# Kernel tuning notes

Measured on AMD Instinct MI355X. Metric: run time of the kernel, lower is better.

Reference implementation:

```python
import jax, jax.numpy as jnp
import numpy as np

BETA = 0.25


def setup_inputs() -> dict:
    key = jax.random.key(0)
    k1, k2 = jax.random.split(key)
    z = jax.random.normal(k1, (16, 1024, 256), dtype=jnp.float32)
    embedding = jax.random.normal(k2, (8192, 256), dtype=jnp.float32)
    return {"z": z, "embedding": embedding}


def reference(z, embedding):
    e_dim = embedding.shape[-1]
    z_flat = jnp.reshape(z, (-1, e_dim))  # [N, e_dim]
    # d[i,k] = ||z_i||^2 + ||e_k||^2 - 2 z_i . e_k  -> [N, n_e]
    d = (jnp.sum(z_flat ** 2, axis=1, keepdims=True)
         + jnp.sum(embedding ** 2, axis=1)
         - 2.0 * jnp.einsum('nd,kd->nk', z_flat, embedding))
    min_encoding_indices = jnp.argmin(d, axis=1)  # [N]
    z_q = embedding[min_encoding_indices]
    z_q = jnp.reshape(z_q, z.shape)
    loss = (jnp.mean((jax.lax.stop_gradient(z_q) - z) ** 2)
            + BETA * jnp.mean((z_q - jax.lax.stop_gradient(z)) ** 2))
    z_q = z + jax.lax.stop_gradient(z_q - z)  # straight-through estimator
    return (z_q, loss, min_encoding_indices)
```

## Files before the change

kernel.cpp:

```cpp
#include <hip/hip_runtime.h>
#include <stdint.h>

#define N_ROWS   16384
#define DIM      256
#define N_CODES  8192
#define ZQ_ELEMS 4194304

typedef _Float16 f16x8 __attribute__((ext_vector_type(8)));
typedef _Float16 f16x4 __attribute__((ext_vector_type(4)));
typedef float    f32x16 __attribute__((ext_vector_type(16)));
typedef unsigned long long u64;

#define WS_ET  0
#define WS_PK  (8650752)

static __device__ __forceinline__ void glds16(const void* gsrc, void* ldst) {
    __builtin_amdgcn_global_load_lds(
        (const __attribute__((address_space(1))) unsigned int*)gsrc,
        (__attribute__((address_space(3))) unsigned int*)ldst,
        16, 0, 0);
}

static __device__ __forceinline__ u64 packkey(float d, int c) {
    unsigned int u = __float_as_uint(d);
    u ^= ((unsigned int)((int)u >> 31)) | 0x80000000u;
    return ((u64)u << 32) | (unsigned int)c;
}

__global__ void vq_prep(const float* __restrict__ emb, const float* __restrict__ z,
                        _Float16* __restrict__ et, _Float16* __restrict__ zt,
                        float* __restrict__ loss_ptr) {
    __shared__ _Float16 shbuf[32768];
    const int t = threadIdx.x, w = t >> 6, l = t & 63;
    if (blockIdx.x < 2048) {
        if (blockIdx.x == 0 && t == 0) *loss_ptr = 0.0f;
        _Float16 (*lh)[256] = (_Float16(*)[256])shbuf;
        _Float16 (*ll)[256] = (_Float16(*)[256])(shbuf + 1024);
        const int code = blockIdx.x * 4 + w;
        float4 v = *(const float4*)(emb + (size_t)code * DIM + l * 4);
        float xs[4] = {v.x, v.y, v.z, v.w};
        f16x4 hh, lo;
        float s = 0.0f;
        #pragma unroll
        for (int i = 0; i < 4; ++i) {
            _Float16 h = (_Float16)xs[i];
            hh[i] = h;
            lo[i] = (_Float16)(xs[i] - (float)h);
            s += xs[i] * xs[i];
        }
        *(f16x4*)&lh[w][l * 4] = hh;
        *(f16x4*)&ll[w][l * 4] = lo;
        #pragma unroll
        for (int off = 32; off > 0; off >>= 1) s += __shfl_down(s, off, 64);
        if (l == 0) {
            _Float16 nh = (_Float16)s;
            _Float16 nl = (_Float16)(s - (float)nh);
            f16x8 aug, zr;
            #pragma unroll
            for (int i = 0; i < 8; ++i) { aug[i] = (_Float16)0; zr[i] = (_Float16)0; }
            aug[0] = nh; aug[1] = nl;
            *(f16x8*)(et + ((size_t)64 * N_CODES + code) * 8) = aug;
            *(f16x8*)(et + ((size_t)65 * N_CODES + code) * 8) = zr;
        }
        __syncthreads();
        const int p = t >> 7, g = t & 127;
        const int cl = g & 3, fg = g >> 2;
        f16x8 frag = (p == 0) ? *(const f16x8*)&lh[cl][fg * 8]
                              : *(const f16x8*)&ll[cl][fg * 8];
        const size_t slab = (size_t)(p * 32 + fg);
        *(f16x8*)(et + (slab * N_CODES + blockIdx.x * 4 + cl) * 8) = frag;
    } else {
        _Float16 (*ls)[64][256] = (_Float16(*)[64][256])shbuf;
        const int row0 = (blockIdx.x - 2048) * 64;
        #pragma unroll
        for (int j = 0; j < 16; ++j) {
            const int row = w * 16 + j;
            float4 v = *(const float4*)(z + (size_t)(row0 + row) * DIM + l * 4);
            float xs[4] = {v.x, v.y, v.z, v.w};
            f16x4 hh, lo;
            #pragma unroll
            for (int i = 0; i < 4; ++i) {
                const float m2 = -2.0f * xs[i];
                _Float16 h = (_Float16)m2;
                hh[i] = h;
                lo[i] = (_Float16)(m2 - (float)h);
            }
            *(f16x4*)&ls[0][row][l * 4] = hh;
            *(f16x4*)&ls[1][row][l * 4] = lo;
        }
        __syncthreads();
        #pragma unroll
        for (int pass = 0; pass < 16; ++pass) {
            const int slab = pass * 4 + w;
            const int p = slab >> 5, fg = slab & 31;
            f16x8 frag = *(const f16x8*)&ls[p][l][fg * 8];
            *(f16x8*)(zt + ((size_t)slab * N_ROWS + row0 + l) * 8) = frag;
        }
    }
}

__global__ __launch_bounds__(512, 2)
void vq_main(const _Float16* __restrict__ zt, const _Float16* __restrict__ et,
             u64* __restrict__ pkeys) {
    extern __shared__ char smem[];
    _Float16* zs = (_Float16*)smem;
    u64* run = (u64*)(smem + 131072);

    const int tid = threadIdx.x;
    const int w = tid >> 6, L = tid & 63, lo5 = L & 31, hi1 = L >> 5;
    const int rb = blockIdx.x >> 1, sp = blockIdx.x & 1;
    const int row0 = rb * 128, codeS = sp * 4096;

    #pragma unroll
    for (int i = 0; i < 16; ++i) {
        const int idx = w * 16 + i;
        const int slab = idx >> 1, half = idx & 1;
        glds16(zt + ((size_t)slab * N_ROWS + row0 + half * 64 + L) * 8,
               smem + ((slab * 128 + half * 64 + L) << 4));
    }
    run[tid] = ~0ULL;
    run[tid + 512] = ~0ULL;
    __syncthreads();

    f16x8 bz;
    #pragma unroll
    for (int i = 0; i < 8; ++i) bz[i] = (_Float16)0;
    if (hi1 == 0) { bz[0] = (_Float16)1; bz[1] = (_Float16)1; }

    for (int ci = 0; ci < 8; ++ci) {
        const int c0 = codeS + ci * 512 + w * 64;

        f16x8 paug[2];
        #pragma unroll
        for (int mt = 0; mt < 2; ++mt)
            paug[mt] = *(const f16x8*)(et +
                ((size_t)(64 + hi1) * N_CODES + c0 + mt * 32 + lo5) * 8);

        f32x16 acc[2][4];
        #pragma unroll
        for (int mt = 0; mt < 2; ++mt)
            #pragma unroll
            for (int nt = 0; nt < 4; ++nt)
                #pragma unroll
                for (int e = 0; e < 16; ++e) acc[mt][nt][e] = 0.0f;

        #pragma unroll 4
        for (int ksg = 0; ksg < 16; ++ksg) {
            const int fg = 2 * ksg + hi1;
            f16x8 ah[2], al[2];
            #pragma unroll
            for (int mt = 0; mt < 2; ++mt) {
                const size_t ao = ((size_t)fg * N_CODES + c0 + mt * 32 + lo5) * 8;
                ah[mt] = *(const f16x8*)(et + ao);
                al[mt] = *(const f16x8*)(et + ao + (size_t)(32 * N_CODES) * 8);
            }
            f16x8 bh[4], bl[4];
            #pragma unroll
            for (int nt = 0; nt < 4; ++nt) {
                const int ro = nt * 32 + lo5;
                bh[nt] = *(const f16x8*)(zs + (size_t)(fg * 128 + ro) * 8);
                bl[nt] = *(const f16x8*)(zs + (size_t)((fg + 32) * 128 + ro) * 8);
            }
            #pragma unroll
            for (int mt = 0; mt < 2; ++mt)
                #pragma unroll
                for (int nt = 0; nt < 4; ++nt) {
                    acc[mt][nt] = __builtin_amdgcn_mfma_f32_32x32x16_f16(ah[mt], bh[nt], acc[mt][nt], 0, 0, 0);
                    acc[mt][nt] = __builtin_amdgcn_mfma_f32_32x32x16_f16(ah[mt], bl[nt], acc[mt][nt], 0, 0, 0);
                    acc[mt][nt] = __builtin_amdgcn_mfma_f32_32x32x16_f16(al[mt], bh[nt], acc[mt][nt], 0, 0, 0);
                }
        }
        #pragma unroll
        for (int mt = 0; mt < 2; ++mt)
            #pragma unroll
            for (int nt = 0; nt < 4; ++nt)
                acc[mt][nt] = __builtin_amdgcn_mfma_f32_32x32x16_f16(paug[mt], bz, acc[mt][nt], 0, 0, 0);

        #pragma unroll
        for (int nt = 0; nt < 4; ++nt) {
            u64 best = ~0ULL;
            #pragma unroll
            for (int mt = 0; mt < 2; ++mt) {
                const int cb = c0 + mt * 32 + 4 * hi1;
                #pragma unroll
                for (int r = 0; r < 16; ++r) {
                    const u64 k = packkey(acc[mt][nt][r],
                                          cb + (r & 3) + 8 * (r >> 2));
                    if (k < best) best = k;
                }
            }
            const u64 o = __shfl_xor(best, 32, 64);
            if (o < best) best = o;
            if (hi1 == 0) {
                u64* p = &run[w * 128 + nt * 32 + lo5];
                if (best < *p) *p = best;
            }
        }
    }

    __syncthreads();
    if (tid < 128) {
        u64 k = run[tid];
        #pragma unroll
        for (int w2 = 1; w2 < 8; ++w2) { u64 o = run[w2 * 128 + tid]; if (o < k) k = o; }
        pkeys[(size_t)sp * N_ROWS + row0 + tid] = k;
    }
}

__global__ __launch_bounds__(512)
void vq_final(const float* __restrict__ z, const float* __restrict__ emb,
              const u64* __restrict__ pkeys,
              float* __restrict__ zq_out, float* __restrict__ loss_out,
              float* __restrict__ idx_out) {
    __shared__ int best[64];
    const int t = threadIdx.x;
    const int row0 = blockIdx.x * 64;
    if (t < 64) {
        u64 k = pkeys[row0 + t];
        u64 o = pkeys[(size_t)N_ROWS + row0 + t];
        if (o < k) k = o;
        const int code = (int)(k & 0xFFFFFFFFu);
        best[t] = code;
        idx_out[row0 + t] = (float)code;
    }
    __syncthreads();
    const int wave = t >> 6, lane = t & 63;
    float lsum = 0.0f;
    #pragma unroll
    for (int rr = 0; rr < 8; ++rr) {
        const int rl = wave * 8 + rr;
        const int rg = row0 + rl;
        const int code = best[rl];
        float4 ev = *(const float4*)(emb + (size_t)code * DIM + lane * 4);
        float4 zv = *(const float4*)(z   + (size_t)rg   * DIM + lane * 4);
        float dx = ev.x - zv.x, dy = ev.y - zv.y;
        float dz = ev.z - zv.z, dw = ev.w - zv.w;
        lsum += dx * dx + dy * dy + dz * dz + dw * dw;
        *(float4*)(zq_out + (size_t)rg * DIM + lane * 4) = ev;
    }
    #pragma unroll
    for (int off = 32; off > 0; off >>= 1) lsum += __shfl_down(lsum, off, 64);
    if (lane == 0) atomicAdd(loss_out, lsum * (1.25f / (float)ZQ_ELEMS));
}

extern "C" void kernel_launch(void* const* d_in, const int* in_sizes, int n_in,
                              void* d_out, int out_size, void* d_ws, size_t ws_size,
                              hipStream_t stream) {
    const float* z   = (const float*)d_in[0];
    const float* emb = (const float*)d_in[1];
    float* out  = (float*)d_out;
    float* zq   = out;
    float* loss = out + ZQ_ELEMS;
    float* idx  = out + ZQ_ELEMS + 1;

    char* ws = (char*)d_ws;
    _Float16* et = (_Float16*)(ws + WS_ET);
    u64*   pk    = (u64*)(ws + WS_PK);

    _Float16* zt = (_Float16*)zq;

    static bool attr_set = false;
    if (!attr_set) {
        hipFuncSetAttribute((const void*)vq_main,
                            hipFuncAttributeMaxDynamicSharedMemorySize, 139264);
        attr_set = true;
    }

    vq_prep<<<2304, 256, 0, stream>>>(emb, z, et, zt, loss);
    vq_main<<<256, 512, 139264, stream>>>(zt, et, pk);
    vq_final<<<N_ROWS / 64, 512, 0, stream>>>(z, emb, pk, zq, loss, idx);
}
```

Baseline: 291.9 us.

## Interleave fp16 operand layout for coalesced loads and streamline argmin epilogue

```diff
diff --git a/kernel.cpp b/kernel.cpp
--- a/kernel.cpp
+++ b/kernel.cpp
@@ -30,12 +30,12 @@
 __global__ void vq_prep(const float* __restrict__ emb, const float* __restrict__ z,
                         _Float16* __restrict__ et, _Float16* __restrict__ zt,
                         float* __restrict__ loss_ptr) {
-    __shared__ _Float16 shbuf[32768];
+    __shared__ _Float16 shbuf[16896];
     const int t = threadIdx.x, w = t >> 6, l = t & 63;
     if (blockIdx.x < 2048) {
         if (blockIdx.x == 0 && t == 0) *loss_ptr = 0.0f;
-        _Float16 (*lh)[256] = (_Float16(*)[256])shbuf;
-        _Float16 (*ll)[256] = (_Float16(*)[256])(shbuf + 1024);
+        _Float16 (*lh)[264] = (_Float16(*)[264])shbuf;
+        _Float16 (*ll)[264] = (_Float16(*)[264])(shbuf + 1056);
         const int code = blockIdx.x * 4 + w;
         float4 v = *(const float4*)(emb + (size_t)code * DIM + l * 4);
         float xs[4] = {v.x, v.y, v.z, v.w};
@@ -59,22 +59,23 @@
             #pragma unroll
             for (int i = 0; i < 8; ++i) { aug[i] = (_Float16)0; zr[i] = (_Float16)0; }
             aug[0] = nh; aug[1] = nl;
-            *(f16x8*)(et + ((size_t)64 * N_CODES + code) * 8) = aug;
-            *(f16x8*)(et + ((size_t)65 * N_CODES + code) * 8) = zr;
+            *(f16x8*)(et + ((size_t)524288 + code) * 8) = aug;
+            *(f16x8*)(et + ((size_t)532480 + code) * 8) = zr;
         }
         __syncthreads();
         const int p = t >> 7, g = t & 127;
         const int cl = g & 3, fg = g >> 2;
         f16x8 frag = (p == 0) ? *(const f16x8*)&lh[cl][fg * 8]
                               : *(const f16x8*)&ll[cl][fg * 8];
-        const size_t slab = (size_t)(p * 32 + fg);
-        *(f16x8*)(et + (slab * N_CODES + blockIdx.x * 4 + cl) * 8) = frag;
+        const size_t unit = (size_t)p * 262144 + (size_t)(fg >> 1) * 16384
+                          + (size_t)(blockIdx.x * 4 + cl) * 2 + (fg & 1);
+        *(f16x8*)(et + unit * 8) = frag;
     } else {
-        _Float16 (*ls)[64][256] = (_Float16(*)[64][256])shbuf;
-        const int row0 = (blockIdx.x - 2048) * 64;
-        #pragma unroll
-        for (int j = 0; j < 16; ++j) {
-            const int row = w * 16 + j;
+        _Float16 (*ls)[32][264] = (_Float16(*)[32][264])shbuf;
+        const int row0 = (blockIdx.x - 2048) * 32;
+        #pragma unroll
+        for (int j = 0; j < 8; ++j) {
+            const int row = w * 8 + j;
             float4 v = *(const float4*)(z + (size_t)(row0 + row) * DIM + l * 4);
             float xs[4] = {v.x, v.y, v.z, v.w};
             f16x4 hh, lo;
@@ -90,11 +91,15 @@
         }
         __syncthreads();
         #pragma unroll
-        for (int pass = 0; pass < 16; ++pass) {
-            const int slab = pass * 4 + w;
-            const int p = slab >> 5, fg = slab & 31;
-            f16x8 frag = *(const f16x8*)&ls[p][l][fg * 8];
-            *(f16x8*)(zt + ((size_t)slab * N_ROWS + row0 + l) * 8) = frag;
+        for (int pp = 0; pp < 8; ++pp) {
+            const int gi = pp * 256 + t;
+            const int p = gi >> 10, rem = gi & 1023;
+            const int ksg = rem >> 6, rr = rem & 63;
+            const int row = rr >> 1, h = rr & 1;
+            f16x8 frag = *(const f16x8*)&ls[p][row][(2 * ksg + h) * 8];
+            const size_t unit = (size_t)p * 524288 + (size_t)ksg * 32768
+                              + (size_t)(row0 + row) * 2 + h;
+            *(f16x8*)(zt + unit * 8) = frag;
         }
     }
 }
@@ -103,7 +108,6 @@
 void vq_main(const _Float16* __restrict__ zt, const _Float16* __restrict__ et,
              u64* __restrict__ pkeys) {
     extern __shared__ char smem[];
-    _Float16* zs = (_Float16*)smem;
     u64* run = (u64*)(smem + 131072);
 
     const int tid = threadIdx.x;
@@ -113,10 +117,11 @@
 
     #pragma unroll
     for (int i = 0; i < 16; ++i) {
-        const int idx = w * 16 + i;
-        const int slab = idx >> 1, half = idx & 1;
-        glds16(zt + ((size_t)slab * N_ROWS + row0 + half * 64 + L) * 8,
-               smem + ((slab * 128 + half * 64 + L) << 4));
+        const int c = w * 16 + i;
+        const int pl = c >> 6, cc = c & 63;
+        glds16(zt + ((size_t)pl * 524288 + (size_t)(cc >> 2) * 32768
+                     + (size_t)row0 * 2 + (cc & 3) * 64 + L) * 8,
+               smem + ((c * 64 + L) << 4));
     }
     run[tid] = ~0ULL;
     run[tid + 512] = ~0ULL;
@@ -127,40 +132,55 @@
     for (int i = 0; i < 8; ++i) bz[i] = (_Float16)0;
     if (hi1 == 0) { bz[0] = (_Float16)1; bz[1] = (_Float16)1; }
 
+    f32x16 zacc;
+    #pragma unroll
+    for (int e = 0; e < 16; ++e) zacc[e] = 0.0f;
+
+    const f16x8* eb  = (const f16x8*)et;
+    const f16x8* ebL = eb + 262144;
+    const int laneU = lo5 * 2 + hi1;
+    const char* zbH = smem + (lo5 * 32 + hi1 * 16);
+    const char* zbL = zbH + 65536;
+
+    f16x8 paug[2];
+    {
+        const int c0 = codeS + w * 64;
+        paug[0] = eb[(size_t)(64 + hi1) * 8192 + c0 + lo5];
+        paug[1] = eb[(size_t)(64 + hi1) * 8192 + c0 + 32 + lo5];
+    }
+
     for (int ci = 0; ci < 8; ++ci) {
         const int c0 = codeS + ci * 512 + w * 64;
-
-        f16x8 paug[2];
+        f32x16 acc[2][4];
+
+        __builtin_amdgcn_s_setprio(1);
         #pragma unroll
         for (int mt = 0; mt < 2; ++mt)
-            paug[mt] = *(const f16x8*)(et +
-                ((size_t)(64 + hi1) * N_CODES + c0 + mt * 32 + lo5) * 8);
-
-        f32x16 acc[2][4];
-        #pragma unroll
-        for (int mt = 0; mt < 2; ++mt)
             #pragma unroll
             for (int nt = 0; nt < 4; ++nt)
-                #pragma unroll
-                for (int e = 0; e < 16; ++e) acc[mt][nt][e] = 0.0f;
-
+                acc[mt][nt] = __builtin_amdgcn_mfma_f32_32x32x16_f16(paug[mt], bz, zacc, 0, 0, 0);
+        __builtin_amdgcn_s_setprio(0);
+
+        if (ci < 7) {
+            const int c1 = codeS + (ci + 1) * 512 + w * 64;
+            paug[0] = eb[(size_t)(64 + hi1) * 8192 + c1 + lo5];
+            paug[1] = eb[(size_t)(64 + hi1) * 8192 + c1 + 32 + lo5];
+        }
+
+        const size_t cu = (size_t)c0 * 2 + laneU;
         #pragma unroll 4
         for (int ksg = 0; ksg < 16; ++ksg) {
-            const int fg = 2 * ksg + hi1;
+            const size_t ub = (size_t)ksg * 16384 + cu;
             f16x8 ah[2], al[2];
-            #pragma unroll
-            for (int mt = 0; mt < 2; ++mt) {
-                const size_t ao = ((size_t)fg * N_CODES + c0 + mt * 32 + lo5) * 8;
-                ah[mt] = *(const f16x8*)(et + ao);
-                al[mt] = *(const f16x8*)(et + ao + (size_t)(32 * N_CODES) * 8);
+            ah[0] = eb[ub];       ah[1] = eb[ub + 64];
+            al[0] = ebL[ub];      al[1] = ebL[ub + 64];
+            f16x8 bh[4], bl[4];
+            #pragma unroll
+            for (int nt = 0; nt < 4; ++nt) {
+                bh[nt] = *(const f16x8*)(zbH + (ksg * 4096 + nt * 1024));
+                bl[nt] = *(const f16x8*)(zbL + (ksg * 4096 + nt * 1024));
             }
-            f16x8 bh[4], bl[4];
-            #pragma unroll
-            for (int nt = 0; nt < 4; ++nt) {
-                const int ro = nt * 32 + lo5;
-                bh[nt] = *(const f16x8*)(zs + (size_t)(fg * 128 + ro) * 8);
-                bl[nt] = *(const f16x8*)(zs + (size_t)((fg + 32) * 128 + ro) * 8);
-            }
+            __builtin_amdgcn_s_setprio(1);
             #pragma unroll
             for (int mt = 0; mt < 2; ++mt)
                 #pragma unroll
@@ -169,26 +189,31 @@
                     acc[mt][nt] = __builtin_amdgcn_mfma_f32_32x32x16_f16(ah[mt], bl[nt], acc[mt][nt], 0, 0, 0);
                     acc[mt][nt] = __builtin_amdgcn_mfma_f32_32x32x16_f16(al[mt], bh[nt], acc[mt][nt], 0, 0, 0);
                 }
-        }
-        #pragma unroll
-        for (int mt = 0; mt < 2; ++mt)
-            #pragma unroll
-            for (int nt = 0; nt < 4; ++nt)
-                acc[mt][nt] = __builtin_amdgcn_mfma_f32_32x32x16_f16(paug[mt], bz, acc[mt][nt], 0, 0, 0);
+            __builtin_amdgcn_s_setprio(0);
+        }
 
         #pragma unroll
         for (int nt = 0; nt < 4; ++nt) {
-            u64 best = ~0ULL;
-            #pragma unroll
-            for (int mt = 0; mt < 2; ++mt) {
-                const int cb = c0 + mt * 32 + 4 * hi1;
+            float mm[16];
+            #pragma unroll
+            for (int r = 0; r < 16; ++r)
+                mm[r] = fminf(acc[0][nt][r], acc[1][nt][r]);
+            #pragma unroll
+            for (int s2 = 8; s2 > 0; s2 >>= 1)
+                #pragma unroll
+                for (int r = 0; r < 8; ++r)
+                    if (r < s2) mm[r] = fminf(mm[r], mm[r + s2]);
+            const float m = mm[0];
+            int rel = 64;
+            #pragma unroll
+            for (int mt = 0; mt < 2; ++mt)
                 #pragma unroll
                 for (int r = 0; r < 16; ++r) {
-                    const u64 k = packkey(acc[mt][nt][r],
-                                          cb + (r & 3) + 8 * (r >> 2));
-                    if (k < best) best = k;
+                    const int rc = mt * 32 + (r & 3) + 8 * (r >> 2);
+                    const int cand = (acc[mt][nt][r] == m) ? rc : 64;
+                    rel = cand < rel ? cand : rel;
                 }
-            }
+            u64 best = packkey(m, c0 + 4 * hi1 + rel);
             const u64 o = __shfl_xor(best, 32, 64);
             if (o < best) best = o;
             if (hi1 == 0) {
@@ -266,7 +291,7 @@
         attr_set = true;
     }
 
-    vq_prep<<<2304, 256, 0, stream>>>(emb, z, et, zt, loss);
+    vq_prep<<<2560, 256, 0, stream>>>(emb, z, et, zt, loss);
     vq_main<<<256, 512, 139264, stream>>>(zt, et, pk);
     vq_final<<<N_ROWS / 64, 512, 0, stream>>>(z, emb, pk, zq, loss, idx);
 }
```

New measurement: 278.9 us. -4.5%, faster.
